# Performance work log

Hardware: AMD Instinct MI355X
Metric: run time of the kernel (lower is better)

## Reference

```python
import jax, jax.numpy as jnp
import numpy as np
import math

N, D_IN, D_OUT = 65536, 512, 512

def setup_inputs() -> dict:
    key = jax.random.key(0)
    k1, k2 = jax.random.split(key)
    x = jax.random.normal(k1, (N, D_IN), dtype=jnp.float32)
    stdv = 1.0 / math.sqrt(D_OUT)
    W = jax.random.uniform(k2, (D_OUT, D_IN), dtype=jnp.float32, minval=-stdv, maxval=stdv)
    W = W.at[:, 0].set(0.0)  # reset_parameters zeroes column 0 (step == in_features)
    b = jnp.zeros((D_OUT,), dtype=jnp.float32)
    scale = jnp.asarray(math.log(10.0), dtype=jnp.float32)  # learned log-scale param
    return {"x": x, "W": W, "b": b, "scale": scale}

def reference(x, W, b, scale):
    # Linear (dropout is identity at inference; nonlin is None)
    y = jnp.einsum('ni,oi->no', x, W) + b               # [N, D_OUT]
    time = jax.nn.sigmoid(y[..., :1]) * jnp.exp(scale) + 1.1   # [N, 1]
    x_narrow = y[..., 1:]                               # [N, D_OUT-1]
    denom = jnp.clip(jnp.sum(x_narrow * x_narrow, axis=-1, keepdims=True), 1e-8, None)
    s = (time * time - 1.0) / denom                     # [N, 1]
    return jnp.concatenate([time, x_narrow * jnp.sqrt(s)], axis=-1)
```

## Files before the change

### kernel.cpp

```cpp
#include <hip/hip_runtime.h>
#include <stdint.h>


typedef short short8 __attribute__((ext_vector_type(8)));
typedef float f32x16 __attribute__((ext_vector_type(16)));
typedef unsigned short ushort4v __attribute__((ext_vector_type(4)));

#define THREADS 512
#define BM 64
#define WTILE 16384
#define XTILE 2048
#define PHASE (WTILE + XTILE)

__device__ __forceinline__ unsigned short f2bf(float f) {
  union { float f; uint32_t u; } v; v.f = f;
  uint32_t u = v.u;
  return (unsigned short)((u + 0x7FFFu + ((u >> 16) & 1u)) >> 16);
}

__device__ __forceinline__ void gload_lds16(const void* g, void* l) {
  __builtin_amdgcn_global_load_lds(
      (const __attribute__((address_space(1))) void*)g,
      (__attribute__((address_space(3))) void*)l, 16, 0, 0);
}

__global__ void wconv_kernel(const float* __restrict__ w,
                             unsigned short* __restrict__ wb) {
  const int i = (blockIdx.x * blockDim.x + threadIdx.x) * 4;
  float4 f = *(const float4*)(w + i);
  ushort4v h;
  h[0] = f2bf(f.x); h[1] = f2bf(f.y); h[2] = f2bf(f.z); h[3] = f2bf(f.w);
  *(ushort4v*)(wb + i) = h;
}

__global__ __launch_bounds__(THREADS, 4) void lorentz_kernel(
    const float* __restrict__ xg, const unsigned short* __restrict__ wb,
    const float* __restrict__ bg, const float* __restrict__ sg,
    float* __restrict__ out) {
  __shared__ __align__(16) char smem[3 * PHASE];
  const int t = threadIdx.x;
  const int lane = t & 63;
  const int wid = t >> 6;
  const int wm = wid >> 2;
  const int wn = wid & 3;
  const int l31 = lane & 31;
  const int h = lane >> 5;
  const int bm = blockIdx.x * BM;

  char* const P0 = smem;
  char* const P1 = smem + PHASE;
  char* const P2 = smem + 2 * PHASE;

  const unsigned short* wsrc0 = wb + (t >> 1) * 512 + (t & 1) * 8;
  const float* xsrc0 = xg + (size_t)(bm + (t >> 3)) * 512 + (t & 7) * 2;
  const int wdst = t * 16;
  const int xdst = WTILE + (t >> 3) * 32 + (t & 7) * 4;
  const int aoff = WTILE + wm * 1024 + l31 * 32 + h * 16;
  const int boff = (wn * 128 + l31) * 32 + h * 16;

  f32x16 acc[4];
  #pragma unroll
  for (int n = 0; n < 4; ++n)
    #pragma unroll
    for (int j = 0; j < 16; ++j) acc[n][j] = 0.f;

  {
    float2 xv0 = *(const float2*)(xsrc0);
    gload_lds16(wsrc0, P0 + wdst);
    gload_lds16(wsrc0 + 131072, P0 + 8192 + wdst);
    unsigned int p0 = (unsigned int)f2bf(xv0.x) | ((unsigned int)f2bf(xv0.y) << 16);
    *(unsigned int*)(P0 + xdst) = p0;
    float2 xv1 = *(const float2*)(xsrc0 + 16);
    gload_lds16(wsrc0 + 16, P1 + wdst);
    gload_lds16(wsrc0 + 16 + 131072, P1 + 8192 + wdst);
    unsigned int p1 = (unsigned int)f2bf(xv1.x) | ((unsigned int)f2bf(xv1.y) << 16);
    *(unsigned int*)(P1 + xdst) = p1;
    asm volatile("s_waitcnt vmcnt(0) lgkmcnt(0)" ::: "memory");
    __builtin_amdgcn_s_barrier();
  }

  auto body = [&](int kt, char* cur, char* nxt, bool drain) {
    short8 af  = *(const short8*)(cur + aoff);
    short8 bf0 = *(const short8*)(cur + boff);
    short8 bf1 = *(const short8*)(cur + boff + 1024);
    short8 bf2 = *(const short8*)(cur + boff + 2048);
    short8 bf3 = *(const short8*)(cur + boff + 3072);
    float2 xv;
    if (nxt) {
      xv = *(const float2*)(xsrc0 + (kt + 2) * 16);
      gload_lds16(wsrc0 + (kt + 2) * 16, nxt + wdst);
      gload_lds16(wsrc0 + (kt + 2) * 16 + 131072, nxt + 8192 + wdst);
    }
    __builtin_amdgcn_s_setprio(1);
    acc[0] = __builtin_amdgcn_mfma_f32_32x32x16_bf16(af, bf0, acc[0], 0, 0, 0);
    acc[1] = __builtin_amdgcn_mfma_f32_32x32x16_bf16(af, bf1, acc[1], 0, 0, 0);
    acc[2] = __builtin_amdgcn_mfma_f32_32x32x16_bf16(af, bf2, acc[2], 0, 0, 0);
    acc[3] = __builtin_amdgcn_mfma_f32_32x32x16_bf16(af, bf3, acc[3], 0, 0, 0);
    __builtin_amdgcn_s_setprio(0);
    if (nxt) {
      unsigned int p = (unsigned int)f2bf(xv.x) | ((unsigned int)f2bf(xv.y) << 16);
      *(unsigned int*)(nxt + xdst) = p;
    }
    if (drain)
      asm volatile("s_waitcnt vmcnt(0) lgkmcnt(0)" ::: "memory");
    else
      asm volatile("s_waitcnt lgkmcnt(0)" ::: "memory");
    __builtin_amdgcn_s_barrier();
  };

  for (int kt = 0; kt < 30; kt += 3) {
    body(kt,     P0, P2, false);
    body(kt + 1, P1, P0, false);
    body(kt + 2, P2, P1, false);
  }
  body(30, P0, nullptr, true);
  body(31, P1, nullptr, false);

  const float esc = __expf(sg[0]);
  float bv[4];
  #pragma unroll
  for (int nr = 0; nr < 4; ++nr) bv[nr] = bg[wn * 128 + nr * 32 + l31];
  #pragma unroll
  for (int nr = 0; nr < 4; ++nr)
    #pragma unroll
    for (int j = 0; j < 16; ++j)
      acc[nr][j] += bv[nr];

  const bool c0 = (wn == 0) && (l31 == 0);
  float ss[16];
  #pragma unroll
  for (int j = 0; j < 16; ++j) {
    float s = 0.f;
    #pragma unroll
    for (int nr = 0; nr < 4; ++nr) { const float v = acc[nr][j]; s += v * v; }
    if (c0) { const float v = acc[0][j]; s -= v * v; }
    ss[j] = s;
  }
  #pragma unroll
  for (int m = 1; m < 32; m <<= 1)
    #pragma unroll
    for (int j = 0; j < 16; ++j)
      ss[j] += __shfl_xor(ss[j], m, 64);

  float* red = (float*)smem;
  float* tsh = (float*)(smem + 256);
  if (t < 64) red[t] = 0.f;
  __syncthreads();
  if (l31 == 0) {
    #pragma unroll
    for (int j = 0; j < 16; ++j) {
      const int r = wm * 32 + (j & 3) + 8 * (j >> 2) + 4 * h;
      atomicAdd(&red[r], ss[j]);
    }
  }
  if (c0) {
    #pragma unroll
    for (int j = 0; j < 16; ++j) {
      const int r = wm * 32 + (j & 3) + 8 * (j >> 2) + 4 * h;
      const float y0 = acc[0][j];
      tsh[r] = esc / (1.f + __expf(-y0)) + 1.1f;
    }
  }
  __syncthreads();

  #pragma unroll
  for (int g = 0; g < 4; ++g) {
    const int rbase = wm * 32 + 8 * g + 4 * h;
    const float4 r4 = *(const float4*)(red + rbase);
    const float4 t4 = *(const float4*)(tsh + rbase);
    #pragma unroll
    for (int j = 0; j < 4; ++j) {
      float denom = (&r4.x)[j];
      denom = denom < 1e-8f ? 1e-8f : denom;
      const float tt = (&t4.x)[j];
      const float coef = sqrtf((tt * tt - 1.f) / denom);
      float* orow = out + (size_t)(bm + rbase + j) * 512;
      #pragma unroll
      for (int nr = 0; nr < 4; ++nr) {
        const int c = wn * 128 + nr * 32 + l31;
        orow[c] = (c == 0) ? tt : acc[nr][4 * g + j] * coef;
      }
    }
  }
}

extern "C" void kernel_launch(void* const* d_in, const int* in_sizes, int n_in,
                              void* d_out, int out_size, void* d_ws, size_t ws_size,
                              hipStream_t stream) {
  const float* x = (const float*)d_in[0];
  const float* W = (const float*)d_in[1];
  const float* b = (const float*)d_in[2];
  const float* sc = (const float*)d_in[3];
  float* outp = (float*)d_out;
  unsigned short* wb = (unsigned short*)d_ws;

  wconv_kernel<<<256, 256, 0, stream>>>(W, wb);
  lorentz_kernel<<<65536 / BM, THREADS, 0, stream>>>(x, wb, b, sc, outp);
}
```

Measured before the change: 308.0 us.

## Retile GEMM to 2x2 MFMA per wave with K=32 double-buffered stages

```diff
diff --git a/kernel.cpp b/kernel.cpp
--- a/kernel.cpp
+++ b/kernel.cpp
@@ -8,8 +8,10 @@
 
 #define THREADS 512
 #define BM 64
-#define WTILE 16384
-#define XTILE 2048
+#define KTILES 16
+#define WTILE 32768
+#define XPAD 1056
+#define XTILE (4 * XPAD)
 #define PHASE (WTILE + XTILE)
 
 __device__ __forceinline__ unsigned short f2bf(float f) {
@@ -37,110 +39,122 @@
     const float* __restrict__ xg, const unsigned short* __restrict__ wb,
     const float* __restrict__ bg, const float* __restrict__ sg,
     float* __restrict__ out) {
-  __shared__ __align__(16) char smem[3 * PHASE];
+  __shared__ __align__(16) char smem[2 * PHASE];
   const int t = threadIdx.x;
   const int lane = t & 63;
-  const int wid = t >> 6;
-  const int wm = wid >> 2;
-  const int wn = wid & 3;
+  const int wn = t >> 6;
   const int l31 = lane & 31;
   const int h = lane >> 5;
   const int bm = blockIdx.x * BM;
 
-  char* const P0 = smem;
-  char* const P1 = smem + PHASE;
-  char* const P2 = smem + 2 * PHASE;
-
-  const unsigned short* wsrc0 = wb + (t >> 1) * 512 + (t & 1) * 8;
-  const float* xsrc0 = xg + (size_t)(bm + (t >> 3)) * 512 + (t & 7) * 2;
+  char* const B0 = smem;
+  char* const B1 = smem + PHASE;
+
+  const unsigned short* wsrc0 = wb + t * 512;
   const int wdst = t * 16;
-  const int xdst = WTILE + (t >> 3) * 32 + (t & 7) * 4;
-  const int aoff = WTILE + wm * 1024 + l31 * 32 + h * 16;
-  const int boff = (wn * 128 + l31) * 32 + h * 16;
-
-  f32x16 acc[4];
-  #pragma unroll
-  for (int n = 0; n < 4; ++n)
-    #pragma unroll
-    for (int j = 0; j < 16; ++j) acc[n][j] = 0.f;
+  const float* xsrc0 = xg + (size_t)(bm + (t >> 3)) * 512 + (t & 7) * 4;
+  const int xdst = ((t & 7) >> 1) * XPAD + (t >> 3) * 16 + (t & 1) * 8;
+  const int abase = h * XPAD + l31 * 16;
+  const int bbase = h * 8192 + (wn * 64 + l31) * 16;
+
+  f32x16 acc[2][2];
+  #pragma unroll
+  for (int a = 0; a < 2; ++a)
+    #pragma unroll
+    for (int n = 0; n < 2; ++n)
+      #pragma unroll
+      for (int j = 0; j < 16; ++j) acc[a][n][j] = 0.f;
+
+  float4 xrA, xrB;
 
   {
-    float2 xv0 = *(const float2*)(xsrc0);
-    gload_lds16(wsrc0, P0 + wdst);
-    gload_lds16(wsrc0 + 131072, P0 + 8192 + wdst);
-    unsigned int p0 = (unsigned int)f2bf(xv0.x) | ((unsigned int)f2bf(xv0.y) << 16);
-    *(unsigned int*)(P0 + xdst) = p0;
-    float2 xv1 = *(const float2*)(xsrc0 + 16);
-    gload_lds16(wsrc0 + 16, P1 + wdst);
-    gload_lds16(wsrc0 + 16 + 131072, P1 + 8192 + wdst);
-    unsigned int p1 = (unsigned int)f2bf(xv1.x) | ((unsigned int)f2bf(xv1.y) << 16);
-    *(unsigned int*)(P1 + xdst) = p1;
-    asm volatile("s_waitcnt vmcnt(0) lgkmcnt(0)" ::: "memory");
+    float4 x0 = *(const float4*)(xsrc0);
+    #pragma unroll
+    for (int i = 0; i < 4; ++i)
+      gload_lds16(wsrc0 + i * 8, B0 + i * 8192 + wdst);
+    uint2 p;
+    p.x = (uint32_t)f2bf(x0.x) | ((uint32_t)f2bf(x0.y) << 16);
+    p.y = (uint32_t)f2bf(x0.z) | ((uint32_t)f2bf(x0.w) << 16);
+    *(uint2*)(B0 + WTILE + xdst) = p;
+    xrB = *(const float4*)(xsrc0 + 32);
+    asm volatile("s_waitcnt vmcnt(1) lgkmcnt(0)" ::: "memory");
     __builtin_amdgcn_s_barrier();
   }
 
-  auto body = [&](int kt, char* cur, char* nxt, bool drain) {
-    short8 af  = *(const short8*)(cur + aoff);
-    short8 bf0 = *(const short8*)(cur + boff);
-    short8 bf1 = *(const short8*)(cur + boff + 1024);
-    short8 bf2 = *(const short8*)(cur + boff + 2048);
-    short8 bf3 = *(const short8*)(cur + boff + 3072);
-    float2 xv;
-    if (nxt) {
-      xv = *(const float2*)(xsrc0 + (kt + 2) * 16);
-      gload_lds16(wsrc0 + (kt + 2) * 16, nxt + wdst);
-      gload_lds16(wsrc0 + (kt + 2) * 16 + 131072, nxt + 8192 + wdst);
-    }
+  auto body = [&](int kt, char* cur, char* nxt, float4& xr_issue,
+                  float4& xr_cvt) {
+    if (kt < 15) {
+      const unsigned short* ws = wsrc0 + (kt + 1) * 32;
+      #pragma unroll
+      for (int i = 0; i < 4; ++i)
+        gload_lds16(ws + i * 8, nxt + i * 8192 + wdst);
+    }
+    if (kt < 14) xr_issue = *(const float4*)(xsrc0 + (kt + 2) * 32);
+    const char* xb = cur + WTILE;
     __builtin_amdgcn_s_setprio(1);
-    acc[0] = __builtin_amdgcn_mfma_f32_32x32x16_bf16(af, bf0, acc[0], 0, 0, 0);
-    acc[1] = __builtin_amdgcn_mfma_f32_32x32x16_bf16(af, bf1, acc[1], 0, 0, 0);
-    acc[2] = __builtin_amdgcn_mfma_f32_32x32x16_bf16(af, bf2, acc[2], 0, 0, 0);
-    acc[3] = __builtin_amdgcn_mfma_f32_32x32x16_bf16(af, bf3, acc[3], 0, 0, 0);
+    #pragma unroll
+    for (int ks = 0; ks < 2; ++ks) {
+      const short8 a0 = *(const short8*)(xb + abase + ks * 2 * XPAD);
+      const short8 a1 = *(const short8*)(xb + abase + ks * 2 * XPAD + 512);
+      const short8 b0 = *(const short8*)(cur + bbase + ks * 16384);
+      const short8 b1 = *(const short8*)(cur + bbase + ks * 16384 + 512);
+      acc[0][0] = __builtin_amdgcn_mfma_f32_32x32x16_bf16(a0, b0, acc[0][0], 0, 0, 0);
+      acc[0][1] = __builtin_amdgcn_mfma_f32_32x32x16_bf16(a0, b1, acc[0][1], 0, 0, 0);
+      acc[1][0] = __builtin_amdgcn_mfma_f32_32x32x16_bf16(a1, b0, acc[1][0], 0, 0, 0);
+      acc[1][1] = __builtin_amdgcn_mfma_f32_32x32x16_bf16(a1, b1, acc[1][1], 0, 0, 0);
+    }
     __builtin_amdgcn_s_setprio(0);
-    if (nxt) {
-      unsigned int p = (unsigned int)f2bf(xv.x) | ((unsigned int)f2bf(xv.y) << 16);
-      *(unsigned int*)(nxt + xdst) = p;
-    }
-    if (drain)
+    if (kt < 15) {
+      uint2 p;
+      p.x = (uint32_t)f2bf(xr_cvt.x) | ((uint32_t)f2bf(xr_cvt.y) << 16);
+      p.y = (uint32_t)f2bf(xr_cvt.z) | ((uint32_t)f2bf(xr_cvt.w) << 16);
+      *(uint2*)(nxt + WTILE + xdst) = p;
+    }
+    if (kt < 14)
+      asm volatile("s_waitcnt vmcnt(1) lgkmcnt(0)" ::: "memory");
+    else if (kt == 14)
       asm volatile("s_waitcnt vmcnt(0) lgkmcnt(0)" ::: "memory");
     else
       asm volatile("s_waitcnt lgkmcnt(0)" ::: "memory");
-    __builtin_amdgcn_s_barrier();
+    if (kt < 15) __builtin_amdgcn_s_barrier();
   };
 
-  for (int kt = 0; kt < 30; kt += 3) {
-    body(kt,     P0, P2, false);
-    body(kt + 1, P1, P0, false);
-    body(kt + 2, P2, P1, false);
-  }
-  body(30, P0, nullptr, true);
-  body(31, P1, nullptr, false);
+  for (int k2 = 0; k2 < KTILES; k2 += 2) {
+    body(k2, B0, B1, xrA, xrB);
+    body(k2 + 1, B1, B0, xrB, xrA);
+  }
 
   const float esc = __expf(sg[0]);
-  float bv[4];
-  #pragma unroll
-  for (int nr = 0; nr < 4; ++nr) bv[nr] = bg[wn * 128 + nr * 32 + l31];
-  #pragma unroll
-  for (int nr = 0; nr < 4; ++nr)
-    #pragma unroll
-    for (int j = 0; j < 16; ++j)
-      acc[nr][j] += bv[nr];
+  float bv[2];
+  #pragma unroll
+  for (int nr = 0; nr < 2; ++nr) bv[nr] = bg[wn * 64 + nr * 32 + l31];
+  #pragma unroll
+  for (int mr = 0; mr < 2; ++mr)
+    #pragma unroll
+    for (int nr = 0; nr < 2; ++nr)
+      #pragma unroll
+      for (int j = 0; j < 16; ++j)
+        acc[mr][nr][j] += bv[nr];
 
   const bool c0 = (wn == 0) && (l31 == 0);
-  float ss[16];
-  #pragma unroll
-  for (int j = 0; j < 16; ++j) {
-    float s = 0.f;
-    #pragma unroll
-    for (int nr = 0; nr < 4; ++nr) { const float v = acc[nr][j]; s += v * v; }
-    if (c0) { const float v = acc[0][j]; s -= v * v; }
-    ss[j] = s;
-  }
+  float ss[2][16];
+  #pragma unroll
+  for (int mr = 0; mr < 2; ++mr)
+    #pragma unroll
+    for (int j = 0; j < 16; ++j) {
+      float s = 0.f;
+      #pragma unroll
+      for (int nr = 0; nr < 2; ++nr) { const float v = acc[mr][nr][j]; s += v * v; }
+      if (c0) { const float v = acc[mr][0][j]; s -= v * v; }
+      ss[mr][j] = s;
+    }
   #pragma unroll
   for (int m = 1; m < 32; m <<= 1)
     #pragma unroll
-    for (int j = 0; j < 16; ++j)
-      ss[j] += __shfl_xor(ss[j], m, 64);
+    for (int mr = 0; mr < 2; ++mr)
+      #pragma unroll
+      for (int j = 0; j < 16; ++j)
+        ss[mr][j] += __shfl_xor(ss[mr][j], m, 64);
 
   float* red = (float*)smem;
   float* tsh = (float*)(smem + 256);
@@ -148,40 +162,46 @@
   __syncthreads();
   if (l31 == 0) {
     #pragma unroll
-    for (int j = 0; j < 16; ++j) {
-      const int r = wm * 32 + (j & 3) + 8 * (j >> 2) + 4 * h;
-      atomicAdd(&red[r], ss[j]);
-    }
+    for (int mr = 0; mr < 2; ++mr)
+      #pragma unroll
+      for (int j = 0; j < 16; ++j) {
+        const int r = mr * 32 + (j & 3) + 8 * (j >> 2) + 4 * h;
+        atomicAdd(&red[r], ss[mr][j]);
+      }
   }
   if (c0) {
     #pragma unroll
-    for (int j = 0; j < 16; ++j) {
-      const int r = wm * 32 + (j & 3) + 8 * (j >> 2) + 4 * h;
-      const float y0 = acc[0][j];
-      tsh[r] = esc / (1.f + __expf(-y0)) + 1.1f;
-    }
+    for (int mr = 0; mr < 2; ++mr)
+      #pragma unroll
+      for (int j = 0; j < 16; ++j) {
+        const int r = mr * 32 + (j & 3) + 8 * (j >> 2) + 4 * h;
+        const float y0 = acc[mr][0][j];
+        tsh[r] = esc / (1.f + __expf(-y0)) + 1.1f;
+      }
   }
   __syncthreads();
 
   #pragma unroll
-  for (int g = 0; g < 4; ++g) {
-    const int rbase = wm * 32 + 8 * g + 4 * h;
-    const float4 r4 = *(const float4*)(red + rbase);
-    const float4 t4 = *(const float4*)(tsh + rbase);
-    #pragma unroll
-    for (int j = 0; j < 4; ++j) {
-      float denom = (&r4.x)[j];
-      denom = denom < 1e-8f ? 1e-8f : denom;
-      const float tt = (&t4.x)[j];
-      const float coef = sqrtf((tt * tt - 1.f) / denom);
-      float* orow = out + (size_t)(bm + rbase + j) * 512;
-      #pragma unroll
-      for (int nr = 0; nr < 4; ++nr) {
-        const int c = wn * 128 + nr * 32 + l31;
-        orow[c] = (c == 0) ? tt : acc[nr][4 * g + j] * coef;
+  for (int mr = 0; mr < 2; ++mr)
+    #pragma unroll
+    for (int g = 0; g < 4; ++g) {
+      const int rbase = mr * 32 + 8 * g + 4 * h;
+      const float4 r4 = *(const float4*)(red + rbase);
+      const float4 t4 = *(const float4*)(tsh + rbase);
+      #pragma unroll
+      for (int j = 0; j < 4; ++j) {
+        float denom = (&r4.x)[j];
+        denom = denom < 1e-8f ? 1e-8f : denom;
+        const float tt = (&t4.x)[j];
+        const float coef = sqrtf((tt * tt - 1.f) / denom);
+        float* orow = out + (size_t)(bm + rbase + j) * 512;
+        #pragma unroll
+        for (int nr = 0; nr < 2; ++nr) {
+          const int c = wn * 64 + nr * 32 + l31;
+          orow[c] = (c == 0) ? tt : acc[mr][nr][4 * g + j] * coef;
+        }
       }
     }
-  }
 }
 
 extern "C" void kernel_launch(void* const* d_in, const int* in_sizes, int n_in,
```

Result: slower. 350.9 us (+13.9%).
